# Kernel optimization log

Hardware: AMD Instinct MI355X
Metric: run time of the kernel (lower is better)

The kernel has to match this reference:

```python
import jax, jax.numpy as jnp
import numpy as np

N_NODES = 100000
IN_C, HID_C, OUT_C = 128, 64, 5
NEG_SLOPE = 0.01  # F.leaky_relu default


def gcn_conv(x, W, b, src_sl, dst_sl, norm, n_nodes):
    """PyG GCNConv: h = D^{-1/2}(A+I)D^{-1/2} (x W) + b.
    src_sl/dst_sl already include self-loops; norm is the per-edge coefficient."""
    h = x @ W                              # [N, out]
    msg = h[src_sl] * norm[:, None]        # [E+N, out] gather + scale
    agg = jax.ops.segment_sum(msg, dst_sl, num_segments=n_nodes)
    return agg + b


def setup_inputs() -> dict:
    key = jax.random.key(0)
    ks = jax.random.split(key, 8)
    n, e = N_NODES, 1600000
    x = jax.random.normal(ks[0], (n, IN_C), dtype=jnp.float32)
    edge_index = jax.random.randint(ks[1], (2, e), 0, n, dtype=jnp.int64)
    idx = jax.random.randint(ks[2], (20000,), 0, n, dtype=jnp.int64)
    # Glorot-ish init for GCNConv weights, kaiming-ish for MLP
    W0 = jax.random.normal(ks[3], (IN_C, HID_C), dtype=jnp.float32) * (1.0 / np.sqrt(IN_C))
    b0 = jnp.zeros((HID_C,), dtype=jnp.float32)
    W1 = jax.random.normal(ks[4], (HID_C, HID_C), dtype=jnp.float32) * (1.0 / np.sqrt(HID_C))
    b1 = jnp.zeros((HID_C,), dtype=jnp.float32)
    Wm = jax.random.normal(ks[5], (HID_C, OUT_C), dtype=jnp.float32) * (1.0 / np.sqrt(HID_C))
    bm = jnp.zeros((OUT_C,), dtype=jnp.float32)
    return {"x": x, "edge_index": edge_index, "idx": idx,
            "W0": W0, "b0": b0, "W1": W1, "b1": b1, "Wm": Wm, "bm": bm}


def reference(x, edge_index, idx, W0, b0, W1, b1, Wm, bm):
    n = x.shape[0]
    src, dst = edge_index[0], edge_index[1]
    loops = jnp.arange(n, dtype=edge_index.dtype)
    src_sl = jnp.concatenate([src, loops])
    dst_sl = jnp.concatenate([dst, loops])
    # symmetric normalization with self-loops (gcn_norm)
    deg = jax.ops.segment_sum(jnp.ones_like(dst_sl, dtype=x.dtype), dst_sl, num_segments=n)
    dinv = jnp.where(deg > 0, jax.lax.rsqrt(deg), 0.0)
    norm = dinv[src_sl] * dinv[dst_sl]     # [E+N]

    h = jax.nn.leaky_relu(gcn_conv(x, W0, b0, src_sl, dst_sl, norm, n), NEG_SLOPE)
    h = jax.nn.leaky_relu(gcn_conv(h, W1, b1, src_sl, dst_sl, norm, n), NEG_SLOPE)

    h_sel = h[idx]                          # index_select on node dim
    out = jax.nn.sigmoid(h_sel @ Wm + bm)
    return (h_sel, out)
```

## Files before the change

kernel.cpp:

```cpp
#include <hip/hip_runtime.h>
#include <hip/hip_fp16.h>
#include <math.h>


#define NPART 64
#define MAXB 2048

typedef _Float16 h8 __attribute__((ext_vector_type(8)));
typedef float f4v __attribute__((ext_vector_type(4)));

__device__ __forceinline__ float lrelu(float x) { return x > 0.0f ? x : 0.01f * x; }


__global__ __launch_bounds__(1024) void k_part_hist(const int* __restrict__ dst, int E,
                                                    int B, int* __restrict__ phist) {
    __shared__ int scnt[MAXB];
    int t = threadIdx.x, p = blockIdx.x;
    for (int i = t; i < B; i += 1024) scnt[i] = 0;
    __syncthreads();
    int ep = (((E + NPART - 1) / NPART) + 3) & ~3;
    int beg = p * ep, endi = min(E, beg + ep);
    int cnt4 = (endi - beg) >> 2;
    for (int i = t; i < cnt4; i += 1024) {
        int4 d = *(const int4*)(dst + beg + i * 4);
        atomicAdd(&scnt[d.x >> 6], 1);
        atomicAdd(&scnt[d.y >> 6], 1);
        atomicAdd(&scnt[d.z >> 6], 1);
        atomicAdd(&scnt[d.w >> 6], 1);
    }
    int rem = (endi - beg) & 3;
    if (t < rem) atomicAdd(&scnt[dst[beg + cnt4 * 4 + t] >> 6], 1);
    __syncthreads();
    for (int i = t; i < B; i += 1024) phist[i * NPART + p] = scnt[i];
}

__global__ __launch_bounds__(1024) void k_part_scatter(const int* __restrict__ src,
                                                       const int* __restrict__ dst, int E,
                                                       int B, const int* __restrict__ pbase,
                                                       int* __restrict__ esA) {
    __shared__ int sbase[MAXB];
    int t = threadIdx.x, p = blockIdx.x;
    for (int i = t; i < B; i += 1024) sbase[i] = pbase[i * NPART + p];
    __syncthreads();
    int ep = (((E + NPART - 1) / NPART) + 3) & ~3;
    int beg = p * ep, endi = min(E, beg + ep);
    int cnt4 = (endi - beg) >> 2;
    for (int i = t; i < cnt4; i += 1024) {
        int e = beg + i * 4;
        int4 d = *(const int4*)(dst + e);
        int4 s = *(const int4*)(src + e);
        int p0 = atomicAdd(&sbase[d.x >> 6], 1);
        int p1 = atomicAdd(&sbase[d.y >> 6], 1);
        int p2 = atomicAdd(&sbase[d.z >> 6], 1);
        int p3 = atomicAdd(&sbase[d.w >> 6], 1);
        esA[p0] = ((d.x & 63) << 24) | s.x;
        esA[p1] = ((d.y & 63) << 24) | s.y;
        esA[p2] = ((d.z & 63) << 24) | s.z;
        esA[p3] = ((d.w & 63) << 24) | s.w;
    }
    int rem = (endi - beg) & 3;
    if (t < rem) {
        int e = beg + cnt4 * 4 + t;
        int d = dst[e];
        int pos = atomicAdd(&sbase[d >> 6], 1);
        esA[pos] = ((d & 63) << 24) | src[e];
    }
}


__global__ void k_blocksum(const int* __restrict__ cnt, int N, int* __restrict__ bsum) {
    __shared__ int sm[256];
    int b = blockIdx.x, t = threadIdx.x;
    int base = b * 1024 + t * 4;
    int s = 0;
#pragma unroll
    for (int i = 0; i < 4; ++i) { int j = base + i; if (j < N) s += cnt[j]; }
    sm[t] = s; __syncthreads();
    for (int off = 128; off > 0; off >>= 1) {
        if (t < off) sm[t] += sm[t + off];
        __syncthreads();
    }
    if (t == 0) bsum[b] = sm[0];
}

__global__ void k_scan_bsum(int* __restrict__ bsum, int nb, int* __restrict__ offN) {
    __shared__ int sm[1024];
    int t = threadIdx.x;
    int v = (t < nb) ? bsum[t] : 0;
    sm[t] = v; __syncthreads();
    for (int d = 1; d < 1024; d <<= 1) {
        int add = (t >= d) ? sm[t - d] : 0;
        __syncthreads();
        sm[t] += add;
        __syncthreads();
    }
    if (t < nb) bsum[t] = sm[t] - v;
    if (t == nb - 1) *offN = sm[t];
}

__global__ void k_scan_block(const int* __restrict__ cnt, const int* __restrict__ bsum,
                             int* __restrict__ off, int N) {
    __shared__ int sm[256];
    int b = blockIdx.x, t = threadIdx.x;
    int base = b * 1024 + t * 4;
    int v[4];
#pragma unroll
    for (int i = 0; i < 4; ++i) { int j = base + i; v[i] = (j < N) ? cnt[j] : 0; }
    int tsum = v[0] + v[1] + v[2] + v[3];
    sm[t] = tsum; __syncthreads();
    for (int d = 1; d < 256; d <<= 1) {
        int val = (t >= d) ? sm[t - d] : 0;
        __syncthreads();
        sm[t] += val;
        __syncthreads();
    }
    int run = sm[t] - tsum + bsum[b];
#pragma unroll
    for (int i = 0; i < 4; ++i) {
        int j = base + i;
        if (j < N) off[j] = run;
        run += v[i];
    }
}


__global__ __launch_bounds__(256) void k_bsort(const int* __restrict__ pbase, int BP,
                                               const int* __restrict__ esA,
                                               int* __restrict__ esB,
                                               int* __restrict__ off,
                                               float* __restrict__ dinv,
                                               int N, int E) {
    __shared__ int hcnt[64];
    __shared__ int hoff[64];
    int t = threadIdx.x, b = blockIdx.x;
    int start = pbase[b * NPART];
    int endi  = pbase[min((b + 1) * NPART, BP)];
    int cnt = endi - start;

    if (t < 64) hcnt[t] = 0;
    __syncthreads();
    for (int i = t * 4; i < cnt; i += 1024) {
#pragma unroll
        for (int c = 0; c < 4; ++c)
            if (i + c < cnt) atomicAdd(&hcnt[(esA[start + i + c] >> 24) & 63], 1);
    }
    __syncthreads();

    if (t < 64) {
        int c = hcnt[t];
        int v = c;
#pragma unroll
        for (int d = 1; d < 64; d <<= 1) {
            int u = __shfl_up(v, d);
            if (t >= d) v += u;
        }
        int pos = start + (v - c);
        hoff[t] = pos;
        int g = b * 64 + t;
        if (g < N) {
            off[g] = pos;
            dinv[g] = rsqrtf((float)c + 1.0f);
        }
        if (g == N - 1) off[N] = E;
    }
    __syncthreads();
    if (t < 64) hcnt[t] = hoff[t];
    __syncthreads();

    for (int i = t * 4; i < cnt; i += 1024) {
#pragma unroll
        for (int c = 0; c < 4; ++c)
            if (i + c < cnt) {
                int v = esA[start + i + c];
                int pos = atomicAdd(&hcnt[(v >> 24) & 63], 1);
                esB[pos] = v & 0xFFFFFF;
            }
    }
}


template <int K, typename AT>
__global__ __launch_bounds__(256) void k_gemm(const AT* __restrict__ A,
                                              const float* __restrict__ W,
                                              const float* __restrict__ dinv,
                                              __half* __restrict__ hout, int N) {
    constexpr int ASTR = K + 8;
    __shared__ _Float16 a16[64 * ASTR];
    __shared__ _Float16 wt16[64 * ASTR];
    int t = threadIdx.x, lane = t & 63, wv = t >> 6;
    int rowBase = blockIdx.x * 64;

#pragma unroll
    for (int i = 0; i < K / 16; ++i) {
        int g = i * 256 + t;
        int r = g / (K / 4), kq = g % (K / 4);
        int gr = rowBase + r; if (gr >= N) gr = N - 1;
        _Float16* p = a16 + r * ASTR + kq * 4;
        if constexpr (sizeof(AT) == 4) {
            float4 v = *(const float4*)((const float*)A + (size_t)gr * K + kq * 4);
            *(__half2*)(p)     = __floats2half2_rn(v.x, v.y);
            *(__half2*)(p + 2) = __floats2half2_rn(v.z, v.w);
        } else {
            *(uint2*)p = *(const uint2*)((const __half*)A + (size_t)gr * K + kq * 4);
        }
    }
#pragma unroll
    for (int i = 0; i < K / 16; ++i) {
        int g = i * 256 + t;
        int k = g >> 4, nq = g & 15;
        float4 v = *(const float4*)(W + (size_t)k * 64 + nq * 4);
        wt16[(nq * 4 + 0) * ASTR + k] = (_Float16)v.x;
        wt16[(nq * 4 + 1) * ASTR + k] = (_Float16)v.y;
        wt16[(nq * 4 + 2) * ASTR + k] = (_Float16)v.z;
        wt16[(nq * 4 + 3) * ASTR + k] = (_Float16)v.w;
    }
    __syncthreads();

    int m = lane & 15, q = lane >> 4;
    f4v acc[4] = {{0,0,0,0},{0,0,0,0},{0,0,0,0},{0,0,0,0}};
    const _Float16* arow = a16 + (wv * 16 + m) * ASTR + q * 8;
#pragma unroll
    for (int kt = 0; kt < K / 32; ++kt) {
        h8 af = *(const h8*)(arow + kt * 32);
#pragma unroll
        for (int nt = 0; nt < 4; ++nt) {
            h8 bf = *(const h8*)(wt16 + (nt * 16 + m) * ASTR + kt * 32 + q * 8);
            acc[nt] = __builtin_amdgcn_mfma_f32_16x16x32_f16(af, bf, acc[nt], 0, 0, 0);
        }
    }

    int r0 = rowBase + wv * 16 + q * 4;
#pragma unroll
    for (int reg = 0; reg < 4; ++reg) {
        int row = r0 + reg;
        if (row >= N) continue;
        float dv = dinv[row];
#pragma unroll
        for (int nt = 0; nt < 4; ++nt)
            hout[(size_t)row * 64 + nt * 16 + m] = (__half)(acc[nt][reg] * dv);
    }
}


__global__ __launch_bounds__(256) void k_agg1(const int* __restrict__ off,
                                              const int* __restrict__ esB,
                                              const float* __restrict__ dinv,
                                              const __half* __restrict__ hs,
                                              const float* __restrict__ b0,
                                              __half* __restrict__ aout, int N) {
    int lane = threadIdx.x & 63;
    int node = (blockIdx.x * blockDim.x + threadIdx.x) >> 6;
    if (node >= N) return;
    int qt = lane >> 4, l16 = lane & 15;
    int beg = off[node], end = off[node + 1];

    float ax = 0, ay = 0, az = 0, aw = 0;
    auto ld = [&](int s) { return *(const uint2*)(hs + (size_t)s * 64 + l16 * 4); };
    auto acc4 = [&](uint2 u) {
        float2 f0 = __half22float2(*(__half2*)&u.x);
        float2 f1 = __half22float2(*(__half2*)&u.y);
        ax += f0.x; ay += f0.y; az += f1.x; aw += f1.y;
    };
    if (qt == 0) acc4(ld(node));
    int j = beg + qt;
    for (; j + 12 < end; j += 16) {
        int s0 = esB[j], s1 = esB[j + 4], s2 = esB[j + 8], s3 = esB[j + 12];
        uint2 u0 = ld(s0), u1 = ld(s1), u2 = ld(s2), u3 = ld(s3);
        acc4(u0); acc4(u1); acc4(u2); acc4(u3);
    }
    for (; j < end; j += 4) acc4(ld(esB[j]));

#pragma unroll
    for (int d = 16; d <= 32; d <<= 1) {
        ax += __shfl_xor(ax, d); ay += __shfl_xor(ay, d);
        az += __shfl_xor(az, d); aw += __shfl_xor(aw, d);
    }
    if (qt == 0) {
        float dv = dinv[node];
        float4 b = *(const float4*)(b0 + l16 * 4);
        float ox = lrelu(ax * dv + b.x), oy = lrelu(ay * dv + b.y);
        float oz = lrelu(az * dv + b.z), ow = lrelu(aw * dv + b.w);
        uint2 u;
        *(__half2*)&u.x = __floats2half2_rn(ox, oy);
        *(__half2*)&u.y = __floats2half2_rn(oz, ow);
        *(uint2*)(aout + (size_t)node * 64 + l16 * 4) = u;
    }
}


__global__ __launch_bounds__(256) void k_aggout(const int* __restrict__ idx,
                                                const int* __restrict__ off,
                                                const int* __restrict__ esB,
                                                const float* __restrict__ dinv,
                                                const __half* __restrict__ hs,
                                                const float* __restrict__ b1,
                                                const float* __restrict__ Wm,
                                                const float* __restrict__ bm,
                                                float* __restrict__ out, int NSEL) {
    int lane = threadIdx.x & 63;
    int wv = (blockIdx.x * blockDim.x + threadIdx.x) >> 6;
    if (wv >= NSEL) return;
    int node = idx[wv];
    int qt = lane >> 4, l16 = lane & 15;
    int beg = off[node], end = off[node + 1];

    float ax = 0, ay = 0, az = 0, aw = 0;
    auto ld = [&](int s) { return *(const uint2*)(hs + (size_t)s * 64 + l16 * 4); };
    auto acc4 = [&](uint2 u) {
        float2 f0 = __half22float2(*(__half2*)&u.x);
        float2 f1 = __half22float2(*(__half2*)&u.y);
        ax += f0.x; ay += f0.y; az += f1.x; aw += f1.y;
    };
    if (qt == 0) acc4(ld(node));
    int j = beg + qt;
    for (; j + 12 < end; j += 16) {
        int s0 = esB[j], s1 = esB[j + 4], s2 = esB[j + 8], s3 = esB[j + 12];
        uint2 u0 = ld(s0), u1 = ld(s1), u2 = ld(s2), u3 = ld(s3);
        acc4(u0); acc4(u1); acc4(u2); acc4(u3);
    }
    for (; j < end; j += 4) acc4(ld(esB[j]));

#pragma unroll
    for (int d = 16; d <= 32; d <<= 1) {
        ax += __shfl_xor(ax, d); ay += __shfl_xor(ay, d);
        az += __shfl_xor(az, d); aw += __shfl_xor(aw, d);
    }

    float dv = dinv[node];
    float4 b = *(const float4*)(b1 + l16 * 4);
    float4 hsel;
    hsel.x = lrelu(ax * dv + b.x); hsel.y = lrelu(ay * dv + b.y);
    hsel.z = lrelu(az * dv + b.z); hsel.w = lrelu(aw * dv + b.w);
    if (qt == 0) *(float4*)(out + (size_t)wv * 64 + l16 * 4) = hsel;

    const float* wr = Wm + (size_t)(4 * l16) * 5;
#pragma unroll
    for (int o = 0; o < 5; ++o) {
        float p = hsel.x * wr[o] + hsel.y * wr[5 + o] +
                  hsel.z * wr[10 + o] + hsel.w * wr[15 + o];
        p += __shfl_xor(p, 1); p += __shfl_xor(p, 2);
        p += __shfl_xor(p, 4); p += __shfl_xor(p, 8);
        if (lane == 0)
            out[(size_t)NSEL * 64 + (size_t)wv * 5 + o] =
                1.0f / (1.0f + expf(-(p + bm[o])));
    }
}

extern "C" void kernel_launch(void* const* d_in, const int* in_sizes, int n_in,
                              void* d_out, int out_size, void* d_ws, size_t ws_size,
                              hipStream_t stream) {
    const float* x   = (const float*)d_in[0];
    const int*   ei  = (const int*)d_in[1];
    const int*   idx = (const int*)d_in[2];
    const float* W0  = (const float*)d_in[3];
    const float* b0  = (const float*)d_in[4];
    const float* W1  = (const float*)d_in[5];
    const float* b1  = (const float*)d_in[6];
    const float* Wm  = (const float*)d_in[7];
    const float* bm  = (const float*)d_in[8];

    int N    = in_sizes[0] / 128;
    int E    = in_sizes[1] / 2;
    int NSEL = in_sizes[2];
    const int* src = ei;
    const int* dst = ei + E;

    int B  = (N + 63) / 64;
    int BP = B * NPART;

    char* w = (char*)d_ws;
    size_t Na  = ((size_t)N + 1023) & ~(size_t)1023;
    size_t Ea  = ((size_t)E + 1023) & ~(size_t)1023;
    size_t BPa = ((size_t)BP + 1023) & ~(size_t)1023;
    float*  dinv  = (float*)w;                w += Na * 4;
    int*    phist = (int*)w;                  w += BPa * 4;
    int*    pbase = (int*)w;                  w += (BPa + 1024) * 4;
    int*    bsum  = (int*)w;                  w += 1024 * 4;
    int*    off   = (int*)w;                  w += (Na + 1024) * 4;
    int*    esA   = (int*)w;                  w += Ea * 4;
    int*    esB   = (int*)w;                  w += Ea * 4;
    __half* hs16  = (__half*)w;               w += (size_t)N * 64 * 2;
    __half* a16g  = (__half*)w;

    int nbp = (BP + 1023) / 1024;

    k_part_hist<<<NPART, 1024, 0, stream>>>(dst, E, B, phist);
    k_blocksum<<<nbp, 256, 0, stream>>>(phist, BP, bsum);
    k_scan_bsum<<<1, 1024, 0, stream>>>(bsum, nbp, pbase + BP);
    k_scan_block<<<nbp, 256, 0, stream>>>(phist, bsum, pbase, BP);
    k_part_scatter<<<NPART, 1024, 0, stream>>>(src, dst, E, B, pbase, esA);
    k_bsort<<<B, 256, 0, stream>>>(pbase, BP, esA, esB, off, dinv, N, E);

    int gemm_blocks = (N + 63) / 64;
    int agg_blocks  = (N + 3) / 4;

    k_gemm<128, float><<<gemm_blocks, 256, 0, stream>>>(x, W0, dinv, hs16, N);
    k_agg1<<<agg_blocks, 256, 0, stream>>>(off, esB, dinv, hs16, b0, a16g, N);
    k_gemm<64, __half><<<gemm_blocks, 256, 0, stream>>>(a16g, W1, dinv, hs16, N);
    k_aggout<<<(NSEL + 3) / 4, 256, 0, stream>>>(idx, off, esB, dinv, hs16, b1, Wm, bm,
                                                 (float*)d_out, NSEL);
}
```

Measured before the change: 260.1 us.

## Restructure CSR aggregation with coalesced index loads, shuffles and 16-byte gathers

Both aggregation kernels now use 8 edge groups of 8 lanes, each lane gathering 16-byte fp16 chunks, where before it was 4 groups of 16 lanes with 8-byte loads. Each wave loads up to 64 neighbour indices with one coalesced load and hands them out by wave shuffle, keeping up to 8 row gathers in flight per lane. The partition count for the histogram stage also rises from 64 to 256 to spread that phase over more blocks. The price is wasted lanes when degree is low, extra shuffles and one more reduction stage.

Result: slower. 265.5 us (+2.1%).

```diff
diff --git a/kernel.cpp b/kernel.cpp
--- a/kernel.cpp
+++ b/kernel.cpp
@@ -3,7 +3,7 @@
 #include <math.h>
 
 
-#define NPART 64
+#define NPART 256
 #define MAXB 2048
 
 typedef _Float16 h8 __attribute__((ext_vector_type(8)));
@@ -251,39 +251,73 @@
     int lane = threadIdx.x & 63;
     int node = (blockIdx.x * blockDim.x + threadIdx.x) >> 6;
     if (node >= N) return;
-    int qt = lane >> 4, l16 = lane & 15;
+    int eg = lane >> 3, l8 = lane & 7;
     int beg = off[node], end = off[node + 1];
-
-    float ax = 0, ay = 0, az = 0, aw = 0;
-    auto ld = [&](int s) { return *(const uint2*)(hs + (size_t)s * 64 + l16 * 4); };
-    auto acc4 = [&](uint2 u) {
+    float dv = dinv[node];
+    float4 blo = *(const float4*)(b0 + l8 * 8);
+    float4 bhi = *(const float4*)(b0 + l8 * 8 + 4);
+
+    float a0=0,a1=0,a2=0,a3=0,a4=0,a5=0,a6=0,a7=0;
+    auto ld = [&](int s) { return *(const uint4*)(hs + (size_t)s * 64 + l8 * 8); };
+    auto acc8 = [&](uint4 u) {
         float2 f0 = __half22float2(*(__half2*)&u.x);
         float2 f1 = __half22float2(*(__half2*)&u.y);
-        ax += f0.x; ay += f0.y; az += f1.x; aw += f1.y;
+        float2 f2 = __half22float2(*(__half2*)&u.z);
+        float2 f3 = __half22float2(*(__half2*)&u.w);
+        a0 += f0.x; a1 += f0.y; a2 += f1.x; a3 += f1.y;
+        a4 += f2.x; a5 += f2.y; a6 += f3.x; a7 += f3.y;
     };
-    if (qt == 0) acc4(ld(node));
-    int j = beg + qt;
-    for (; j + 12 < end; j += 16) {
-        int s0 = esB[j], s1 = esB[j + 4], s2 = esB[j + 8], s3 = esB[j + 12];
-        uint2 u0 = ld(s0), u1 = ld(s1), u2 = ld(s2), u3 = ld(s3);
-        acc4(u0); acc4(u1); acc4(u2); acc4(u3);
-    }
-    for (; j < end; j += 4) acc4(ld(esB[j]));
-
-#pragma unroll
-    for (int d = 16; d <= 32; d <<= 1) {
-        ax += __shfl_xor(ax, d); ay += __shfl_xor(ay, d);
-        az += __shfl_xor(az, d); aw += __shfl_xor(aw, d);
-    }
-    if (qt == 0) {
-        float dv = dinv[node];
-        float4 b = *(const float4*)(b0 + l16 * 4);
-        float ox = lrelu(ax * dv + b.x), oy = lrelu(ay * dv + b.y);
-        float oz = lrelu(az * dv + b.z), ow = lrelu(aw * dv + b.w);
-        uint2 u;
-        *(__half2*)&u.x = __floats2half2_rn(ox, oy);
-        *(__half2*)&u.y = __floats2half2_rn(oz, ow);
-        *(uint2*)(aout + (size_t)node * 64 + l16 * 4) = u;
+    if (eg == 0) acc8(ld(node));
+
+    for (int base = beg; base < end; base += 64) {
+        int nb = min(end - base, 64);
+        int myIdx = esB[min(base + lane, end - 1)];
+        if (nb <= 16) {
+            int s0 = __shfl(myIdx, min(eg,     nb - 1));
+            int s1 = __shfl(myIdx, min(eg + 8, nb - 1));
+            uint4 u0 = ld(s0), u1 = ld(s1);
+            if (eg     < nb) acc8(u0);
+            if (eg + 8 < nb) acc8(u1);
+        } else {
+            int s0 = __shfl(myIdx, min(eg,      nb - 1));
+            int s1 = __shfl(myIdx, min(eg + 8,  nb - 1));
+            int s2 = __shfl(myIdx, min(eg + 16, nb - 1));
+            int s3 = __shfl(myIdx, min(eg + 24, nb - 1));
+            int s4 = __shfl(myIdx, min(eg + 32, nb - 1));
+            int s5 = __shfl(myIdx, min(eg + 40, nb - 1));
+            int s6 = __shfl(myIdx, min(eg + 48, nb - 1));
+            int s7 = __shfl(myIdx, min(eg + 56, nb - 1));
+            uint4 u0 = ld(s0), u1 = ld(s1), u2 = ld(s2), u3 = ld(s3);
+            uint4 u4 = ld(s4), u5 = ld(s5), u6 = ld(s6), u7 = ld(s7);
+            acc8(u0);
+            acc8(u1);
+            if (eg + 16 < nb) acc8(u2);
+            if (eg + 24 < nb) acc8(u3);
+            if (eg + 32 < nb) acc8(u4);
+            if (eg + 40 < nb) acc8(u5);
+            if (eg + 48 < nb) acc8(u6);
+            if (eg + 56 < nb) acc8(u7);
+        }
+    }
+
+#pragma unroll
+    for (int d = 8; d <= 32; d <<= 1) {
+        a0 += __shfl_xor(a0, d); a1 += __shfl_xor(a1, d);
+        a2 += __shfl_xor(a2, d); a3 += __shfl_xor(a3, d);
+        a4 += __shfl_xor(a4, d); a5 += __shfl_xor(a5, d);
+        a6 += __shfl_xor(a6, d); a7 += __shfl_xor(a7, d);
+    }
+    if (eg == 0) {
+        float o0 = lrelu(a0 * dv + blo.x), o1 = lrelu(a1 * dv + blo.y);
+        float o2 = lrelu(a2 * dv + blo.z), o3 = lrelu(a3 * dv + blo.w);
+        float o4 = lrelu(a4 * dv + bhi.x), o5 = lrelu(a5 * dv + bhi.y);
+        float o6 = lrelu(a6 * dv + bhi.z), o7 = lrelu(a7 * dv + bhi.w);
+        uint4 u;
+        *(__half2*)&u.x = __floats2half2_rn(o0, o1);
+        *(__half2*)&u.y = __floats2half2_rn(o2, o3);
+        *(__half2*)&u.z = __floats2half2_rn(o4, o5);
+        *(__half2*)&u.w = __floats2half2_rn(o6, o7);
+        *(uint4*)(aout + (size_t)node * 64 + l8 * 8) = u;
     }
 }
 
@@ -301,45 +335,80 @@
     int wv = (blockIdx.x * blockDim.x + threadIdx.x) >> 6;
     if (wv >= NSEL) return;
     int node = idx[wv];
-    int qt = lane >> 4, l16 = lane & 15;
+    int eg = lane >> 3, l8 = lane & 7;
     int beg = off[node], end = off[node + 1];
-
-    float ax = 0, ay = 0, az = 0, aw = 0;
-    auto ld = [&](int s) { return *(const uint2*)(hs + (size_t)s * 64 + l16 * 4); };
-    auto acc4 = [&](uint2 u) {
+    float dv = dinv[node];
+    float4 blo = *(const float4*)(b1 + l8 * 8);
+    float4 bhi = *(const float4*)(b1 + l8 * 8 + 4);
+
+    float a0=0,a1=0,a2=0,a3=0,a4=0,a5=0,a6=0,a7=0;
+    auto ld = [&](int s) { return *(const uint4*)(hs + (size_t)s * 64 + l8 * 8); };
+    auto acc8 = [&](uint4 u) {
         float2 f0 = __half22float2(*(__half2*)&u.x);
         float2 f1 = __half22float2(*(__half2*)&u.y);
-        ax += f0.x; ay += f0.y; az += f1.x; aw += f1.y;
+        float2 f2 = __half22float2(*(__half2*)&u.z);
+        float2 f3 = __half22float2(*(__half2*)&u.w);
+        a0 += f0.x; a1 += f0.y; a2 += f1.x; a3 += f1.y;
+        a4 += f2.x; a5 += f2.y; a6 += f3.x; a7 += f3.y;
     };
-    if (qt == 0) acc4(ld(node));
-    int j = beg + qt;
-    for (; j + 12 < end; j += 16) {
-        int s0 = esB[j], s1 = esB[j + 4], s2 = esB[j + 8], s3 = esB[j + 12];
-        uint2 u0 = ld(s0), u1 = ld(s1), u2 = ld(s2), u3 = ld(s3);
-        acc4(u0); acc4(u1); acc4(u2); acc4(u3);
-    }
-    for (; j < end; j += 4) acc4(ld(esB[j]));
-
-#pragma unroll
-    for (int d = 16; d <= 32; d <<= 1) {
-        ax += __shfl_xor(ax, d); ay += __shfl_xor(ay, d);
-        az += __shfl_xor(az, d); aw += __shfl_xor(aw, d);
-    }
-
-    float dv = dinv[node];
-    float4 b = *(const float4*)(b1 + l16 * 4);
-    float4 hsel;
-    hsel.x = lrelu(ax * dv + b.x); hsel.y = lrelu(ay * dv + b.y);
-    hsel.z = lrelu(az * dv + b.z); hsel.w = lrelu(aw * dv + b.w);
-    if (qt == 0) *(float4*)(out + (size_t)wv * 64 + l16 * 4) = hsel;
-
-    const float* wr = Wm + (size_t)(4 * l16) * 5;
+    if (eg == 0) acc8(ld(node));
+
+    for (int base = beg; base < end; base += 64) {
+        int nb = min(end - base, 64);
+        int myIdx = esB[min(base + lane, end - 1)];
+        if (nb <= 16) {
+            int s0 = __shfl(myIdx, min(eg,     nb - 1));
+            int s1 = __shfl(myIdx, min(eg + 8, nb - 1));
+            uint4 u0 = ld(s0), u1 = ld(s1);
+            if (eg     < nb) acc8(u0);
+            if (eg + 8 < nb) acc8(u1);
+        } else {
+            int s0 = __shfl(myIdx, min(eg,      nb - 1));
+            int s1 = __shfl(myIdx, min(eg + 8,  nb - 1));
+            int s2 = __shfl(myIdx, min(eg + 16, nb - 1));
+            int s3 = __shfl(myIdx, min(eg + 24, nb - 1));
+            int s4 = __shfl(myIdx, min(eg + 32, nb - 1));
+            int s5 = __shfl(myIdx, min(eg + 40, nb - 1));
+            int s6 = __shfl(myIdx, min(eg + 48, nb - 1));
+            int s7 = __shfl(myIdx, min(eg + 56, nb - 1));
+            uint4 u0 = ld(s0), u1 = ld(s1), u2 = ld(s2), u3 = ld(s3);
+            uint4 u4 = ld(s4), u5 = ld(s5), u6 = ld(s6), u7 = ld(s7);
+            acc8(u0);
+            acc8(u1);
+            if (eg + 16 < nb) acc8(u2);
+            if (eg + 24 < nb) acc8(u3);
+            if (eg + 32 < nb) acc8(u4);
+            if (eg + 40 < nb) acc8(u5);
+            if (eg + 48 < nb) acc8(u6);
+            if (eg + 56 < nb) acc8(u7);
+        }
+    }
+
+#pragma unroll
+    for (int d = 8; d <= 32; d <<= 1) {
+        a0 += __shfl_xor(a0, d); a1 += __shfl_xor(a1, d);
+        a2 += __shfl_xor(a2, d); a3 += __shfl_xor(a3, d);
+        a4 += __shfl_xor(a4, d); a5 += __shfl_xor(a5, d);
+        a6 += __shfl_xor(a6, d); a7 += __shfl_xor(a7, d);
+    }
+
+    float h0 = lrelu(a0 * dv + blo.x), h1 = lrelu(a1 * dv + blo.y);
+    float h2 = lrelu(a2 * dv + blo.z), h3 = lrelu(a3 * dv + blo.w);
+    float h4 = lrelu(a4 * dv + bhi.x), h5 = lrelu(a5 * dv + bhi.y);
+    float h6 = lrelu(a6 * dv + bhi.z), h7 = lrelu(a7 * dv + bhi.w);
+    if (eg == 0) {
+        float4 w0 = {h0, h1, h2, h3};
+        float4 w1 = {h4, h5, h6, h7};
+        *(float4*)(out + (size_t)wv * 64 + l8 * 8)     = w0;
+        *(float4*)(out + (size_t)wv * 64 + l8 * 8 + 4) = w1;
+    }
+
+    const float* wr = Wm + (size_t)(8 * l8) * 5;
 #pragma unroll
     for (int o = 0; o < 5; ++o) {
-        float p = hsel.x * wr[o] + hsel.y * wr[5 + o] +
-                  hsel.z * wr[10 + o] + hsel.w * wr[15 + o];
-        p += __shfl_xor(p, 1); p += __shfl_xor(p, 2);
-        p += __shfl_xor(p, 4); p += __shfl_xor(p, 8);
+        float p = h0 * wr[o]      + h1 * wr[5 + o]  + h2 * wr[10 + o] + h3 * wr[15 + o] +
+                  h4 * wr[20 + o] + h5 * wr[25 + o] + h6 * wr[30 + o] + h7 * wr[35 + o];
+        p += __shfl_xor(p, 1); p += __shfl_xor(p, 2); p += __shfl_xor(p, 4);
         if (lane == 0)
             out[(size_t)NSEL * 64 + (size_t)wv * 5 + o] =
                 1.0f / (1.0f + expf(-(p + bm[o])));
```
